# Kernel tuning notes

Hardware: AMD Instinct MI355X
Metric: run time of the kernel (lower is better)

The kernel has to match this reference:

```python
import jax, jax.numpy as jnp
import numpy as np

N_NODES = 50000
N_EDGES = 800000
LN_EPS = 1e-5


def _segment_softmax_aggr(msg, t, dst, n):
    # SoftmaxAggregation(learn=True): alpha = softmax(msg * t) per dest segment, out = sum(alpha * msg)
    logits = msg * t  # [E, C]
    m = jax.ops.segment_max(logits, dst, num_segments=n)
    m = jnp.where(jnp.isfinite(m), m, 0.0)  # empty segments -> 0 to keep exp finite
    e = jnp.exp(logits - m[dst])
    denom = jax.ops.segment_sum(e, dst, num_segments=n)
    alpha = e / jnp.maximum(denom[dst], 1e-16)
    return jax.ops.segment_sum(alpha * msg, dst, num_segments=n)


def _sage_conv(x, src, dst, wp, bp, t, wl, bl, wr):
    # project=True: messages come from relu(lin(x)); root term uses ORIGINAL x
    xp = jax.nn.relu(x @ wp + bp)
    msg = xp[src]                                   # [E, C] gather
    aggr = _segment_softmax_aggr(msg, t, dst, x.shape[0])
    out = aggr @ wl + bl + x @ wr
    # normalize=True: L2 normalize rows (eps as in F.normalize)
    nrm = jnp.maximum(jnp.linalg.norm(out, axis=-1, keepdims=True), 1e-12)
    return out / nrm


def _mem_pool(x, k, w_conv, wl, bl):
    # PyG MemPooling, tau=1: Student-t kernel 1/(1+d^2)
    H, K, F = k.shape
    kk = k.reshape(H * K, F)
    d2 = (jnp.sum(kk * kk, -1)[:, None] + jnp.sum(x * x, -1)[None, :]
          - 2.0 * kk @ x.T)                          # [H*K, N]
    d2 = jnp.maximum(d2, 0.0)
    dist = 1.0 / (1.0 + d2)
    dist = dist.reshape(H, K, -1).transpose(0, 2, 1)  # [H, N, K]
    S = dist / jnp.sum(dist, -1, keepdims=True)       # per-head normalize over clusters
    S = jnp.einsum('h,hnk->nk', w_conv, S)            # 1x1 conv mixing heads (no bias)
    S = jax.nn.softmax(S, axis=-1)                    # [N, K]
    xp = S.T @ x                                      # [K, F]
    return xp @ wl + bl                               # [K, out]


def setup_inputs() -> dict:
    key = jax.random.key(0)
    ks = jax.random.split(key, 20)
    rn = lambda i, shp, s: jax.random.normal(ks[i], shp, dtype=jnp.float32) * s
    inp = {
        'x': rn(0, (N_NODES, 64), 1.0),
        'edge_index': jax.random.randint(ks[1], (2, N_EDGES), 0, N_NODES, dtype=jnp.int32),
        'w_proj1': rn(2, (64, 64), 0.1), 'b_proj1': rn(3, (64,), 0.05),
        't1': jnp.ones((64,), jnp.float32),
        'w_l1': rn(4, (64, 256), 0.1), 'b_l1': rn(5, (256,), 0.05),
        'w_r1': rn(6, (64, 256), 0.1),
        'w_proj2': rn(7, (256, 256), 0.05), 'b_proj2': rn(8, (256,), 0.05),
        't2': jnp.ones((256,), jnp.float32),
        'w_l2': rn(9, (256, 128), 0.05), 'b_l2': rn(10, (128,), 0.05),
        'w_r2': rn(11, (256, 128), 0.05),
        'k_mem': rn(12, (4, 4, 128), 1.0),
        'w_conv': rn(13, (4,), 0.5),
        'w_memlin': rn(14, (128, 128), 0.08), 'b_memlin': rn(15, (128,), 0.05),
        'w_fx': rn(16, (128, 64), 0.08), 'b_fx': rn(17, (64,), 0.05),
        'gamma': jnp.ones((64,), jnp.float32),
        'beta': jnp.zeros((64,), jnp.float32),
    }
    return inp


def reference(x, edge_index, w_proj1, b_proj1, t1, w_l1, b_l1, w_r1,
              w_proj2, b_proj2, t2, w_l2, b_l2, w_r2,
              k_mem, w_conv, w_memlin, b_memlin, w_fx, b_fx, gamma, beta):
    src, dst = edge_index[0], edge_index[1]
    h = _sage_conv(x, src, dst, w_proj1, b_proj1, t1, w_l1, b_l1, w_r1)
    h = jax.nn.relu(h)                              # dropout = identity (eval)
    h = _sage_conv(h, src, dst, w_proj2, b_proj2, t2, w_l2, b_l2, w_r2)
    h = jax.nn.relu(h)
    pooled = _mem_pool(h, k_mem, w_conv, w_memlin, b_memlin)  # [4, 128]
    g = jnp.mean(pooled, axis=0, keepdims=True)     # global_mean_pool -> [1, 128]
    y = g @ w_fx + b_fx                             # [1, 64]
    mu = jnp.mean(y, -1, keepdims=True)
    var = jnp.var(y, -1, keepdims=True)
    y = (y - mu) / jnp.sqrt(var + LN_EPS) * gamma + beta
    return jax.nn.relu(y)
```

## Files before the change

### kernel.cpp

```cpp
#include <hip/hip_runtime.h>
#include <hip/hip_bf16.h>

#define N_NODES 50000
#define N_EDGES 800000
#define NB 196
#define PC_SLICES 2048

typedef __attribute__((ext_vector_type(8))) short short8;
typedef __attribute__((ext_vector_type(4))) float f32x4;
typedef __attribute__((ext_vector_type(2))) float f32x2;

#define QSCALE (2.f / 255.f)
#define QINV   127.5f

__device__ __forceinline__ float us2f(unsigned short u) {
    return __uint_as_float(((unsigned int)u) << 16);
}
__device__ __forceinline__ unsigned short f2bu(float f) {
    unsigned int u = __float_as_uint(f);
    unsigned int r = (u + 0x7fffu + ((u >> 16) & 1u)) >> 16;
    return (unsigned short)r;
}
__device__ __forceinline__ float exp2_hw(float x) {
    float r;
    __asm__("v_exp_f32 %0, %1" : "=v"(r) : "v"(x));
    return r;
}
#define LOG2E 1.44269504088896f

__global__ void k_hist(const int* __restrict__ dst, int* __restrict__ counts) {
    int e = blockIdx.x * 256 + threadIdx.x;
    if (e < N_EDGES) atomicAdd(&counts[dst[e]], 1);
}

__global__ __launch_bounds__(256) void k_scan1(const int* __restrict__ counts,
                                               int* __restrict__ row_ptr,
                                               int* __restrict__ partial) {
    __shared__ int sd[256];
    int t = threadIdx.x, i = blockIdx.x * 256 + t;
    int v = (i < N_NODES) ? counts[i] : 0;
    sd[t] = v;
    __syncthreads();
    for (int off = 1; off < 256; off <<= 1) {
        int o = (t >= off) ? sd[t - off] : 0;
        __syncthreads();
        sd[t] += o;
        __syncthreads();
    }
    if (i < N_NODES) row_ptr[i] = sd[t] - v;
    if (t == 255) partial[blockIdx.x] = sd[255];
}

__global__ __launch_bounds__(256) void k_scan2(int* __restrict__ partial,
                                               int* __restrict__ row_ptr) {
    __shared__ int sd[256];
    int t = threadIdx.x;
    int v = (t < NB) ? partial[t] : 0;
    sd[t] = v;
    __syncthreads();
    for (int off = 1; off < 256; off <<= 1) {
        int o = (t >= off) ? sd[t - off] : 0;
        __syncthreads();
        sd[t] += o;
        __syncthreads();
    }
    if (t < NB) partial[t] = sd[t] - v;
    if (t == NB - 1) row_ptr[N_NODES] = sd[t];
}

__global__ __launch_bounds__(256) void k_scan3(int* __restrict__ row_ptr,
                                               const int* __restrict__ partial,
                                               int* __restrict__ cursor) {
    int i = blockIdx.x * 256 + threadIdx.x;
    if (i < N_NODES) {
        int v = row_ptr[i] + partial[blockIdx.x];
        row_ptr[i] = v;
        cursor[i] = v;
    }
}

__global__ void k_scatter(const int* __restrict__ src, const int* __restrict__ dst,
                          int* __restrict__ cursor, int* __restrict__ src_sorted) {
    int e = blockIdx.x * 256 + threadIdx.x;
    if (e < N_EDGES) {
        int d = dst[e];
        int pos = atomicAdd(&cursor[d], 1);
        src_sorted[pos] = src[e];
    }
}

#define XCAST_N (N_NODES * 64)
__global__ __launch_bounds__(256) void k_prep(const float* __restrict__ x,
                                              const float* __restrict__ wp1,
                                              const float* __restrict__ wl1,
                                              const float* __restrict__ wr1,
                                              const float* __restrict__ wp2,
                                              const float* __restrict__ wl2,
                                              const float* __restrict__ wr2,
                                              unsigned short* __restrict__ cat1,
                                              unsigned short* __restrict__ B0T,
                                              unsigned short* __restrict__ B1T,
                                              unsigned short* __restrict__ BP2T,
                                              unsigned short* __restrict__ B2T) {
    int idx = blockIdx.x * 256 + threadIdx.x;
    if (idx < XCAST_N) {
        int i = idx >> 6, j = idx & 63;
        cat1[i * 128 + 64 + j] = f2bu(x[idx]);
        return;
    }
    int w = idx - XCAST_N;
    if (w < 4096)  { int k = w >> 6, n = w & 63;  B0T[n * 64 + k] = f2bu(wp1[w]); return; }
    w -= 4096;
    if (w < 16384) { int k = w >> 8, n = w & 255; B1T[n * 128 + k] = f2bu(wl1[w]); return; }
    w -= 16384;
    if (w < 16384) { int k = w >> 8, n = w & 255; B1T[n * 128 + 64 + k] = f2bu(wr1[w]); return; }
    w -= 16384;
    if (w < 65536) { int k = w >> 8, n = w & 255; BP2T[n * 256 + k] = f2bu(wp2[w]); return; }
    w -= 65536;
    if (w < 32768) { int k = w >> 7, n = w & 127; B2T[n * 512 + k] = f2bu(wl2[w]); return; }
    w -= 32768;
    if (w < 32768) { int k = w >> 7, n = w & 127; B2T[n * 512 + 256 + k] = f2bu(wr2[w]); return; }
}

template<int K, int C, int LDA, int LDOUT, int OUT_OFF, int EP, int WPB>
__global__ __launch_bounds__(256, WPB) void k_gemm(const unsigned short* __restrict__ A,
                                                   const unsigned short* __restrict__ BT,
                                                   const float* __restrict__ bias,
                                                   void* __restrict__ outv) {
    constexpr int NT = C / 16;
    constexpr int SAE = 128 * 72;
    constexpr int SBE = C * 72;
    constexpr int STAGE_B = (SAE + SBE) * 2;
    constexpr int RP_B = 64 * C * (EP == 2 ? 4 : (EP == 3 ? 1 : 2));
    constexpr int SMEM_B = STAGE_B > RP_B ? STAGE_B : RP_B;
    __shared__ __align__(16) char smem[SMEM_B];
    unsigned short* sA = (unsigned short*)smem;
    unsigned short* sB = sA + SAE;

    int t = threadIdx.x;
    int wid = t >> 6, lane = t & 63;
    int lrow = lane & 15, quad = lane >> 4;
    int m0 = blockIdx.x * 128;

    f32x4 acc[2][NT];
#pragma unroll
    for (int h = 0; h < 2; ++h)
#pragma unroll
        for (int nt = 0; nt < NT; ++nt)
#pragma unroll
            for (int r = 0; r < 4; ++r) acc[h][nt][r] = 0.f;

    for (int k0 = 0; k0 < K; k0 += 64) {
        __syncthreads();
        for (int i = t; i < 1024; i += 256) {
            int r = i >> 3, seg = i & 7;
            int m = m0 + r;
            uint4 v = make_uint4(0u, 0u, 0u, 0u);
            if (m < N_NODES) v = *(const uint4*)&A[(size_t)m * LDA + k0 + seg * 8];
            *(uint4*)&sA[r * 72 + seg * 8] = v;
        }
        for (int i = t; i < C * 8; i += 256) {
            int n = i >> 3, seg = i & 7;
            uint4 v = *(const uint4*)&BT[(size_t)n * K + k0 + seg * 8];
            *(uint4*)&sB[n * 72 + seg * 8] = v;
        }
        __syncthreads();
#pragma unroll
        for (int kk = 0; kk < 2; ++kk) {
            short8 a0 = *(const short8*)&sA[(wid * 16 + lrow) * 72 + kk * 32 + quad * 8];
            short8 a1 = *(const short8*)&sA[(64 + wid * 16 + lrow) * 72 + kk * 32 + quad * 8];
#pragma unroll
            for (int nt = 0; nt < NT; ++nt) {
                short8 bfg = *(const short8*)&sB[(nt * 16 + lrow) * 72 + kk * 32 + quad * 8];
                acc[0][nt] = __builtin_amdgcn_mfma_f32_16x16x32_bf16(a0, bfg, acc[0][nt], 0, 0, 0);
                acc[1][nt] = __builtin_amdgcn_mfma_f32_16x16x32_bf16(a1, bfg, acc[1][nt], 0, 0, 0);
            }
        }
    }

#pragma unroll
    for (int h = 0; h < 2; ++h) {
#pragma unroll
        for (int nt = 0; nt < NT; ++nt) {
            float bv = bias[nt * 16 + lrow];
#pragma unroll
            for (int r = 0; r < 4; ++r) acc[h][nt][r] += bv;
        }
        if (EP == 1 || EP == 2) {
#pragma unroll
            for (int r = 0; r < 4; ++r) {
                float ss = 0.f;
#pragma unroll
                for (int nt = 0; nt < NT; ++nt) ss += acc[h][nt][r] * acc[h][nt][r];
                ss += __shfl_xor(ss, 1);
                ss += __shfl_xor(ss, 2);
                ss += __shfl_xor(ss, 4);
                ss += __shfl_xor(ss, 8);
                float rinv = 1.f / fmaxf(sqrtf(ss), 1e-12f);
#pragma unroll
                for (int nt = 0; nt < NT; ++nt)
                    acc[h][nt][r] = fmaxf(acc[h][nt][r] * rinv, 0.f);
            }
        } else {
#pragma unroll
            for (int nt = 0; nt < NT; ++nt)
#pragma unroll
                for (int r = 0; r < 4; ++r) acc[h][nt][r] = fmaxf(acc[h][nt][r], 0.f);
        }
    }

    __syncthreads();
#pragma unroll
    for (int h = 0; h < 2; ++h) {
        if (EP == 2) {
            float* rp = (float*)smem;
#pragma unroll
            for (int nt = 0; nt < NT; ++nt)
#pragma unroll
                for (int r = 0; r < 4; ++r)
                    rp[(wid * 16 + quad * 4 + r) * C + nt * 16 + lrow] = acc[h][nt][r];
            __syncthreads();
            float* outp = (float*)outv;
            for (int i = t; i < 64 * C / 4; i += 256) {
                int f = i * 4, r = f / C, c = f % C;
                int m = m0 + h * 64 + r;
                if (m < N_NODES)
                    *(float4*)&outp[(size_t)m * LDOUT + OUT_OFF + c] = *(const float4*)&rp[f];
            }
            __syncthreads();
        } else if (EP == 3) {
            unsigned char* rp = (unsigned char*)smem;
#pragma unroll
            for (int nt = 0; nt < NT; ++nt)
#pragma unroll
                for (int r = 0; r < 4; ++r) {
                    float q = fminf(__builtin_rintf(acc[h][nt][r] * QINV), 255.f);
                    rp[(wid * 16 + quad * 4 + r) * C + nt * 16 + lrow] = (unsigned char)(int)q;
                }
            __syncthreads();
            unsigned char* outp = (unsigned char*)outv;
            for (int i = t; i < 64 * C / 16; i += 256) {
                int f = i * 16, r = f / C, c = f % C;
                int m = m0 + h * 64 + r;
                if (m < N_NODES)
                    *(uint4*)&outp[(size_t)m * LDOUT + OUT_OFF + c] = *(const uint4*)&rp[f];
            }
            __syncthreads();
        } else {
            unsigned short* rp = (unsigned short*)smem;
#pragma unroll
            for (int nt = 0; nt < NT; ++nt)
#pragma unroll
                for (int r = 0; r < 4; ++r)
                    rp[(wid * 16 + quad * 4 + r) * C + nt * 16 + lrow] = f2bu(acc[h][nt][r]);
            __syncthreads();
            unsigned short* outp = (unsigned short*)outv;
            for (int i = t; i < 64 * C / 8; i += 256) {
                int f = i * 8, r = f / C, c = f % C;
                int m = m0 + h * 64 + r;
                if (m < N_NODES)
                    *(uint4*)&outp[(size_t)m * LDOUT + OUT_OFF + c] = *(const uint4*)&rp[f];
            }
            __syncthreads();
        }
    }
}

__global__ __launch_bounds__(64) void k_aggr256(const unsigned char* __restrict__ xp,
                                                const float* __restrict__ tvec,
                                                const int* __restrict__ row_ptr,
                                                const int* __restrict__ srcs,
                                                unsigned short* __restrict__ outp) {
    int t = threadIdx.x;
    float4 tv4 = *(const float4*)&tvec[t * 4];
    f32x2 tv01 = {tv4.x * (LOG2E * QSCALE), tv4.y * (LOG2E * QSCALE)};
    f32x2 tv23 = {tv4.z * (LOG2E * QSCALE), tv4.w * (LOG2E * QSCALE)};
    int n = blockIdx.x;
    int beg = row_ptr[n], end = row_ptr[n + 1];
    f32x2 se01 = {0.f, 0.f}, se23 = {0.f, 0.f};
    f32x2 sem01 = {0.f, 0.f}, sem23 = {0.f, 0.f};
    int e = beg;
#define EDGE_BODY(VV, MSK)                                                     \
    {                                                                          \
        f32x2 m01 = {(float)((VV) & 0xFFu), (float)(((VV) >> 8) & 0xFFu)};     \
        f32x2 m23 = {(float)(((VV) >> 16) & 0xFFu), (float)((VV) >> 24)};      \
        f32x2 l01 = m01 * tv01, l23 = m23 * tv23;                              \
        f32x2 w01, w23;                                                        \
        w01.x = exp2_hw(l01.x) * (MSK); w01.y = exp2_hw(l01.y) * (MSK);        \
        w23.x = exp2_hw(l23.x) * (MSK); w23.y = exp2_hw(l23.y) * (MSK);        \
        se01 += w01; se23 += w23;                                              \
        sem01 = __builtin_elementwise_fma(w01, m01, sem01);                    \
        sem23 = __builtin_elementwise_fma(w23, m23, sem23);                    \
    }
    for (; e + 16 <= end; e += 16) {
        unsigned int v[16];
#pragma unroll
        for (int j = 0; j < 16; ++j) {
            const unsigned char* p = xp + (size_t)srcs[e + j] * 256;
            v[j] = *(const unsigned int*)&p[t * 4];
        }
#pragma unroll
        for (int j = 0; j < 16; ++j) EDGE_BODY(v[j], 1.f)
    }
    for (; e + 8 <= end; e += 8) {
        unsigned int v[8];
#pragma unroll
        for (int j = 0; j < 8; ++j) {
            const unsigned char* p = xp + (size_t)srcs[e + j] * 256;
            v[j] = *(const unsigned int*)&p[t * 4];
        }
#pragma unroll
        for (int j = 0; j < 8; ++j) EDGE_BODY(v[j], 1.f)
    }
    if (e < end) {
        int last = end - 1;
        unsigned int v[8];
#pragma unroll
        for (int j = 0; j < 8; ++j) {
            int ee = e + j;
            ee = ee < end ? ee : last;
            const unsigned char* p = xp + (size_t)srcs[ee] * 256;
            v[j] = *(const unsigned int*)&p[t * 4];
        }
#pragma unroll
        for (int j = 0; j < 8; ++j) {
            float msk = (e + j < end) ? 1.f : 0.f;
            EDGE_BODY(v[j], msk)
        }
    }
#undef EDGE_BODY
    ushort4 o;
    o.x = f2bu(QSCALE * sem01.x / fmaxf(se01.x, 1e-16f));
    o.y = f2bu(QSCALE * sem01.y / fmaxf(se01.y, 1e-16f));
    o.z = f2bu(QSCALE * sem23.x / fmaxf(se23.x, 1e-16f));
    o.w = f2bu(QSCALE * sem23.y / fmaxf(se23.y, 1e-16f));
    *(ushort4*)&outp[(size_t)n * 512 + t * 4] = o;
}

__global__ __launch_bounds__(64) void k_aggr64(const unsigned short* __restrict__ xp,
                                               const float* __restrict__ tvec,
                                               const int* __restrict__ row_ptr,
                                               const int* __restrict__ srcs,
                                               unsigned short* __restrict__ outp) {
    int c = threadIdx.x;
    float tv = tvec[c] * LOG2E;
    int n = blockIdx.x;
    int beg = row_ptr[n], end = row_ptr[n + 1];
    float se = 0.f, sem = 0.f;
    int e = beg;
    for (; e + 16 <= end; e += 16) {
        unsigned short v[16];
#pragma unroll
        for (int j = 0; j < 16; ++j)
            v[j] = xp[(size_t)srcs[e + j] * 64 + c];
#pragma unroll
        for (int j = 0; j < 16; ++j) {
            float msg = us2f(v[j]);
            float w = exp2_hw(msg * tv);
            se += w;
            sem = fmaf(w, msg, sem);
        }
    }
    for (; e + 8 <= end; e += 8) {
        unsigned short v[8];
#pragma unroll
        for (int j = 0; j < 8; ++j)
            v[j] = xp[(size_t)srcs[e + j] * 64 + c];
#pragma unroll
        for (int j = 0; j < 8; ++j) {
            float msg = us2f(v[j]);
            float w = exp2_hw(msg * tv);
            se += w;
            sem = fmaf(w, msg, sem);
        }
    }
    if (e < end) {
        int last = end - 1;
        unsigned short v[8];
#pragma unroll
        for (int j = 0; j < 8; ++j) {
            int ee = e + j;
            ee = ee < end ? ee : last;
            v[j] = xp[(size_t)srcs[ee] * 64 + c];
        }
#pragma unroll
        for (int j = 0; j < 8; ++j) {
            float msk = (e + j < end) ? 1.f : 0.f;
            float msg = us2f(v[j]);
            float w = exp2_hw(msg * tv) * msk;
            se += w;
            sem = fmaf(w, msg, sem);
        }
    }
    outp[(size_t)n * 128 + c] = f2bu(sem / fmaxf(se, 1e-16f));
}

__global__ __launch_bounds__(64) void k_pool_s(const float* __restrict__ h2,
                                               const float* __restrict__ kmem,
                                               const float* __restrict__ wconv,
                                               float* __restrict__ S) {
    __shared__ float kls[2048];
    __shared__ float kk2s[16];
    int t = threadIdx.x;
    for (int i = t; i < 2048; i += 64) kls[i] = kmem[i];
    __syncthreads();
    if (t < 16) {
        float s = 0.f;
        for (int f = 0; f < 128; ++f) { float v = kls[t * 128 + f]; s += v * v; }
        kk2s[t] = s;
    }
    __syncthreads();
    int n = blockIdx.x * 64 + t;
    if (n >= N_NODES) return;
    float dots[16];
#pragma unroll
    for (int k = 0; k < 16; ++k) dots[k] = 0.f;
    float x2 = 0.f;
    for (int c = 0; c < 32; ++c) {
        float4 xv = *(const float4*)&h2[(size_t)n * 128 + c * 4];
        x2 += xv.x * xv.x + xv.y * xv.y + xv.z * xv.z + xv.w * xv.w;
#pragma unroll
        for (int k = 0; k < 16; ++k) {
            float4 kv = *(const float4*)&kls[k * 128 + c * 4];
            dots[k] += xv.x * kv.x + xv.y * kv.y + xv.z * kv.z + xv.w * kv.w;
        }
    }
    float dist[16];
#pragma unroll
    for (int k = 0; k < 16; ++k) {
        float d2 = fmaxf(kk2s[k] + x2 - 2.f * dots[k], 0.f);
        dist[k] = 1.f / (1.f + d2);
    }
    float s0 = 0.f, s1 = 0.f, s2 = 0.f, s3 = 0.f;
#pragma unroll
    for (int h = 0; h < 4; ++h) {
        float den = dist[h * 4] + dist[h * 4 + 1] + dist[h * 4 + 2] + dist[h * 4 + 3];
        float inv = wconv[h] / den;
        s0 += dist[h * 4 + 0] * inv;
        s1 += dist[h * 4 + 1] * inv;
        s2 += dist[h * 4 + 2] * inv;
        s3 += dist[h * 4 + 3] * inv;
    }
    float mx = fmaxf(fmaxf(s0, s1), fmaxf(s2, s3));
    float e0 = __expf(s0 - mx), e1 = __expf(s1 - mx), e2 = __expf(s2 - mx), e3 = __expf(s3 - mx);
    float inv = 1.f / (e0 + e1 + e2 + e3);
    float4 o = make_float4(e0 * inv, e1 * inv, e2 * inv, e3 * inv);
    *(float4*)&S[(size_t)n * 4] = o;
}

__global__ __launch_bounds__(256) void k_pool_c(const float* __restrict__ h2,
                                                const float* __restrict__ Sm,
                                                float* __restrict__ part) {
    int t = threadIdx.x;
    int c = t & 127, sub = t >> 7;
    int slice = blockIdx.x * 2 + sub;
    float a0 = 0.f, a1 = 0.f, a2 = 0.f, a3 = 0.f;
    for (int n = slice; n < N_NODES; n += PC_SLICES) {
        float xv = h2[(size_t)n * 128 + c];
        float4 sv = *(const float4*)&Sm[(size_t)n * 4];
        a0 = fmaf(sv.x, xv, a0);
        a1 = fmaf(sv.y, xv, a1);
        a2 = fmaf(sv.z, xv, a2);
        a3 = fmaf(sv.w, xv, a3);
    }
    float* p = &part[(size_t)slice * 512];
    p[0 * 128 + c] = a0;
    p[1 * 128 + c] = a1;
    p[2 * 128 + c] = a2;
    p[3 * 128 + c] = a3;
}

__global__ __launch_bounds__(256) void k_pool_b(const float* __restrict__ part,
                                                float* __restrict__ pooled) {
    int j = blockIdx.x;
    float s = 0.f;
    for (int b = threadIdx.x; b < PC_SLICES; b += 256) s += part[(size_t)b * 512 + j];
#pragma unroll
    for (int off = 32; off > 0; off >>= 1) s += __shfl_xor(s, off);
    __shared__ float red[4];
    int lane = threadIdx.x & 63, wid = threadIdx.x >> 6;
    if (lane == 0) red[wid] = s;
    __syncthreads();
    if (threadIdx.x == 0) pooled[j] = red[0] + red[1] + red[2] + red[3];
}

__global__ __launch_bounds__(128) void k_final(const float* __restrict__ pooled,
                                               const float* __restrict__ wmem,
                                               const float* __restrict__ bmem,
                                               const float* __restrict__ wfx,
                                               const float* __restrict__ bfx,
                                               const float* __restrict__ gamma,
                                               const float* __restrict__ beta,
                                               float* __restrict__ out) {
    __shared__ float gx[128], g[128];
    int t = threadIdx.x;
    gx[t] = 0.25f * (pooled[t] + pooled[128 + t] + pooled[256 + t] + pooled[384 + t]);
    __syncthreads();
    float acc = bmem[t];
    for (int f = 0; f < 128; ++f) acc = fmaf(gx[f], wmem[f * 128 + t], acc);
    g[t] = acc;
    __syncthreads();
    if (t < 64) {
        float y = bfx[t];
        for (int f = 0; f < 128; ++f) y = fmaf(g[f], wfx[f * 64 + t], y);
        float s = y, s2 = y * y;
#pragma unroll
        for (int off = 32; off > 0; off >>= 1) {
            s += __shfl_xor(s, off);
            s2 += __shfl_xor(s2, off);
        }
        float mu = s * (1.f / 64.f);
        float var = s2 * (1.f / 64.f) - mu * mu;
        float v = (y - mu) / sqrtf(var + 1e-5f) * gamma[t] + beta[t];
        out[t] = fmaxf(v, 0.f);
    }
}

extern "C" void kernel_launch(void* const* d_in, const int* in_sizes, int n_in,
                              void* d_out, int out_size, void* d_ws, size_t ws_size,
                              hipStream_t stream) {
    const float* x        = (const float*)d_in[0];
    const int*   ei       = (const int*)  d_in[1];
    const float* w_proj1  = (const float*)d_in[2];
    const float* b_proj1  = (const float*)d_in[3];
    const float* t1       = (const float*)d_in[4];
    const float* w_l1     = (const float*)d_in[5];
    const float* b_l1     = (const float*)d_in[6];
    const float* w_r1     = (const float*)d_in[7];
    const float* w_proj2  = (const float*)d_in[8];
    const float* b_proj2  = (const float*)d_in[9];
    const float* t2       = (const float*)d_in[10];
    const float* w_l2     = (const float*)d_in[11];
    const float* b_l2     = (const float*)d_in[12];
    const float* w_r2     = (const float*)d_in[13];
    const float* k_mem    = (const float*)d_in[14];
    const float* w_conv   = (const float*)d_in[15];
    const float* w_memlin = (const float*)d_in[16];
    const float* b_memlin = (const float*)d_in[17];
    const float* w_fx     = (const float*)d_in[18];
    const float* b_fx     = (const float*)d_in[19];
    const float* gamma    = (const float*)d_in[20];
    const float* beta     = (const float*)d_in[21];
    const int* src = ei;
    const int* dst = ei + N_EDGES;
    (void)in_sizes; (void)n_in; (void)out_size; (void)ws_size;

    char* W = (char*)d_ws;
    const size_t MB = 1024 * 1024;
    int*   row_ptr    = (int*)(W + 0);
    int*   cursor     = (int*)(W + 256 * 1024);
    int*   partial    = (int*)(W + 512 * 1024);
    int*   src_sorted = (int*)(W + 768 * 1024);
    unsigned short* cat1 = (unsigned short*)(W + 4 * MB);
    unsigned short* xp1  = (unsigned short*)(W + 17 * MB);
    unsigned short* cat2 = (unsigned short*)(W + 24 * MB);
    unsigned char*  xp2  = (unsigned char*)(W + 76 * MB);
    float* h2     = (float*)(W + 102 * MB);
    float* Sm     = (float*)(W + 128 * MB);
    float* pooled = (float*)(W + 131 * MB);
    unsigned short* B0T  = (unsigned short*)(W + 133 * MB);
    unsigned short* B1T  = (unsigned short*)(W + 134 * MB);
    unsigned short* BP2T = (unsigned short*)(W + 135 * MB);
    unsigned short* B2T  = (unsigned short*)(W + 136 * MB);
    float* part   = (float*)(W + 140 * MB);

    hipMemsetAsync(cursor, 0, N_NODES * sizeof(int), stream);
    k_hist<<<(N_EDGES + 255) / 256, 256, 0, stream>>>(dst, cursor);
    k_scan1<<<NB, 256, 0, stream>>>(cursor, row_ptr, partial);
    k_scan2<<<1, 256, 0, stream>>>(partial, row_ptr);
    k_scan3<<<NB, 256, 0, stream>>>(row_ptr, partial, cursor);
    k_scatter<<<(N_EDGES + 255) / 256, 256, 0, stream>>>(src, dst, cursor, src_sorted);

    k_prep<<<(XCAST_N + 167936 + 255) / 256, 256, 0, stream>>>(
        x, w_proj1, w_l1, w_r1, w_proj2, w_l2, w_r2, cat1, B0T, B1T, BP2T, B2T);

    const int GB = (N_NODES + 127) / 128;

    k_gemm<64, 64, 128, 64, 0, 0, 4><<<GB, 256, 0, stream>>>(cat1 + 64, B0T, b_proj1, xp1);
    k_aggr64<<<N_NODES, 64, 0, stream>>>(xp1, t1, row_ptr, src_sorted, cat1);
    k_gemm<128, 256, 128, 512, 256, 1, 2><<<GB, 256, 0, stream>>>(cat1, B1T, b_l1, cat2);

    k_gemm<256, 256, 512, 256, 0, 3, 2><<<GB, 256, 0, stream>>>(cat2 + 256, BP2T, b_proj2, xp2);
    k_aggr256<<<N_NODES, 64, 0, stream>>>(xp2, t2, row_ptr, src_sorted, cat2);
    k_gemm<512, 128, 512, 128, 0, 2, 4><<<GB, 256, 0, stream>>>(cat2, B2T, b_l2, h2);

    k_pool_s<<<(N_NODES + 63) / 64, 64, 0, stream>>>(h2, k_mem, w_conv, Sm);
    k_pool_c<<<PC_SLICES / 2, 256, 0, stream>>>(h2, Sm, part);
    k_pool_b<<<512, 256, 0, stream>>>(part, pooled);
    k_final<<<1, 128, 0, stream>>>(pooled, w_memlin, b_memlin, w_fx, b_fx, gamma, beta,
                                   (float*)d_out);
}
```

Measured before the change: 388.8 us.

## Fuse pooling assignment into final GEMM epilogue and merge scan kernels

Computes the MemPooling soft assignment S directly from the fp32 result tile held in shared memory inside the last GEMM's epilogue. This removes the separate k_pool_s kernel and its full re-read of h2. It also folds the single-block partial scan into the per-block offset kernel, where each block reduces the preceding partial sums itself, and hardcodes the row_ptr tail as N_EDGES. The cost is extra shared memory and a lower occupancy hint (WPB 4 to 3) for that GEMM, plus redundant per-block reductions in the scan.

Result: no change. 385.7 us (-0.8%).

```diff
diff --git a/kernel.cpp b/kernel.cpp
--- a/kernel.cpp
+++ b/kernel.cpp
@@ -51,32 +51,25 @@
     if (t == 255) partial[blockIdx.x] = sd[255];
 }
 
-__global__ __launch_bounds__(256) void k_scan2(int* __restrict__ partial,
-                                               int* __restrict__ row_ptr) {
+__global__ __launch_bounds__(256) void k_scan3b(int* __restrict__ row_ptr,
+                                                const int* __restrict__ partial,
+                                                int* __restrict__ cursor) {
     __shared__ int sd[256];
     int t = threadIdx.x;
-    int v = (t < NB) ? partial[t] : 0;
-    sd[t] = v;
+    sd[t] = (t < blockIdx.x) ? partial[t] : 0;
     __syncthreads();
-    for (int off = 1; off < 256; off <<= 1) {
-        int o = (t >= off) ? sd[t - off] : 0;
+    for (int off = 128; off > 0; off >>= 1) {
+        if (t < off) sd[t] += sd[t + off];
         __syncthreads();
-        sd[t] += o;
-        __syncthreads();
-    }
-    if (t < NB) partial[t] = sd[t] - v;
-    if (t == NB - 1) row_ptr[N_NODES] = sd[t];
-}
-
-__global__ __launch_bounds__(256) void k_scan3(int* __restrict__ row_ptr,
-                                               const int* __restrict__ partial,
-                                               int* __restrict__ cursor) {
-    int i = blockIdx.x * 256 + threadIdx.x;
+    }
+    int base = sd[0];
+    int i = blockIdx.x * 256 + t;
     if (i < N_NODES) {
-        int v = row_ptr[i] + partial[blockIdx.x];
+        int v = row_ptr[i] + base;
         row_ptr[i] = v;
         cursor[i] = v;
     }
+    if (blockIdx.x == 0 && t == 0) row_ptr[N_NODES] = N_EDGES;
 }
 
 __global__ void k_scatter(const int* __restrict__ src, const int* __restrict__ dst,
@@ -126,21 +119,39 @@
 __global__ __launch_bounds__(256, WPB) void k_gemm(const unsigned short* __restrict__ A,
                                                    const unsigned short* __restrict__ BT,
                                                    const float* __restrict__ bias,
-                                                   void* __restrict__ outv) {
+                                                   void* __restrict__ outv,
+                                                   const float* __restrict__ kmem,
+                                                   const float* __restrict__ wconv,
+                                                   float* __restrict__ Sm) {
     constexpr int NT = C / 16;
     constexpr int SAE = 128 * 72;
     constexpr int SBE = C * 72;
     constexpr int STAGE_B = (SAE + SBE) * 2;
     constexpr int RP_B = 64 * C * (EP == 2 ? 4 : (EP == 3 ? 1 : 2));
     constexpr int SMEM_B = STAGE_B > RP_B ? STAGE_B : RP_B;
-    __shared__ __align__(16) char smem[SMEM_B];
+    constexpr int POOL_B = (EP == 2) ? (2048 * 4 + 64 + 16) : 16;
+    __shared__ __align__(16) char smem[SMEM_B + POOL_B];
     unsigned short* sA = (unsigned short*)smem;
     unsigned short* sB = sA + SAE;
+    float* kls  = (float*)(smem + SMEM_B);
+    float* kk2s = kls + 2048;
+    float* wcs  = kk2s + 16;
 
     int t = threadIdx.x;
     int wid = t >> 6, lane = t & 63;
     int lrow = lane & 15, quad = lane >> 4;
     int m0 = blockIdx.x * 128;
+
+    if (EP == 2) {
+        for (int i = t; i < 2048; i += 256) kls[i] = kmem[i];
+        if (t < 4) wcs[t] = wconv[t];
+        __syncthreads();
+        if (t < 16) {
+            float s = 0.f;
+            for (int f = 0; f < 128; ++f) { float v = kls[t * 128 + f]; s += v * v; }
+            kk2s[t] = s;
+        }
+    }
 
     f32x4 acc[2][NT];
 #pragma unroll
@@ -226,6 +237,59 @@
                 int m = m0 + h * 64 + r;
                 if (m < N_NODES)
                     *(float4*)&outp[(size_t)m * LDOUT + OUT_OFF + c] = *(const float4*)&rp[f];
+            }
+            {
+                int row = t >> 2, p = t & 3;
+                int cbase = p * 32;
+                float dots[16];
+#pragma unroll
+                for (int k = 0; k < 16; ++k) dots[k] = 0.f;
+                float x2 = 0.f;
+#pragma unroll
+                for (int c4 = 0; c4 < 8; ++c4) {
+                    float4 xv = *(const float4*)&rp[row * C + cbase + c4 * 4];
+                    x2 += xv.x * xv.x + xv.y * xv.y + xv.z * xv.z + xv.w * xv.w;
+#pragma unroll
+                    for (int k = 0; k < 16; ++k) {
+                        float4 kv = *(const float4*)&kls[k * 128 + cbase + c4 * 4];
+                        dots[k] += xv.x * kv.x + xv.y * kv.y + xv.z * kv.z + xv.w * kv.w;
+                    }
+                }
+#pragma unroll
+                for (int k = 0; k < 16; ++k) {
+                    dots[k] += __shfl_xor(dots[k], 1);
+                    dots[k] += __shfl_xor(dots[k], 2);
+                }
+                x2 += __shfl_xor(x2, 1);
+                x2 += __shfl_xor(x2, 2);
+                if (p == 0) {
+                    int m = m0 + h * 64 + row;
+                    if (m < N_NODES) {
+                        float dist[16];
+#pragma unroll
+                        for (int k = 0; k < 16; ++k) {
+                            float d2 = fmaxf(kk2s[k] + x2 - 2.f * dots[k], 0.f);
+                            dist[k] = 1.f / (1.f + d2);
+                        }
+                        float s0 = 0.f, s1 = 0.f, s2 = 0.f, s3 = 0.f;
+#pragma unroll
+                        for (int hh = 0; hh < 4; ++hh) {
+                            float den = dist[hh * 4] + dist[hh * 4 + 1] +
+                                        dist[hh * 4 + 2] + dist[hh * 4 + 3];
+                            float inv = wcs[hh] / den;
+                            s0 += dist[hh * 4 + 0] * inv;
+                            s1 += dist[hh * 4 + 1] * inv;
+                            s2 += dist[hh * 4 + 2] * inv;
+                            s3 += dist[hh * 4 + 3] * inv;
+                        }
+                        float mx = fmaxf(fmaxf(s0, s1), fmaxf(s2, s3));
+                        float e0 = __expf(s0 - mx), e1 = __expf(s1 - mx);
+                        float e2 = __expf(s2 - mx), e3 = __expf(s3 - mx);
+                        float inv = 1.f / (e0 + e1 + e2 + e3);
+                        *(float4*)&Sm[(size_t)m * 4] =
+                            make_float4(e0 * inv, e1 * inv, e2 * inv, e3 * inv);
+                    }
+                }
             }
             __syncthreads();
         } else if (EP == 3) {
@@ -393,59 +457,6 @@
         }
     }
     outp[(size_t)n * 128 + c] = f2bu(sem / fmaxf(se, 1e-16f));
-}
-
-__global__ __launch_bounds__(64) void k_pool_s(const float* __restrict__ h2,
-                                               const float* __restrict__ kmem,
-                                               const float* __restrict__ wconv,
-                                               float* __restrict__ S) {
-    __shared__ float kls[2048];
-    __shared__ float kk2s[16];
-    int t = threadIdx.x;
-    for (int i = t; i < 2048; i += 64) kls[i] = kmem[i];
-    __syncthreads();
-    if (t < 16) {
-        float s = 0.f;
-        for (int f = 0; f < 128; ++f) { float v = kls[t * 128 + f]; s += v * v; }
-        kk2s[t] = s;
-    }
-    __syncthreads();
-    int n = blockIdx.x * 64 + t;
-    if (n >= N_NODES) return;
-    float dots[16];
-#pragma unroll
-    for (int k = 0; k < 16; ++k) dots[k] = 0.f;
-    float x2 = 0.f;
-    for (int c = 0; c < 32; ++c) {
-        float4 xv = *(const float4*)&h2[(size_t)n * 128 + c * 4];
-        x2 += xv.x * xv.x + xv.y * xv.y + xv.z * xv.z + xv.w * xv.w;
-#pragma unroll
-        for (int k = 0; k < 16; ++k) {
-            float4 kv = *(const float4*)&kls[k * 128 + c * 4];
-            dots[k] += xv.x * kv.x + xv.y * kv.y + xv.z * kv.z + xv.w * kv.w;
-        }
-    }
-    float dist[16];
-#pragma unroll
-    for (int k = 0; k < 16; ++k) {
-        float d2 = fmaxf(kk2s[k] + x2 - 2.f * dots[k], 0.f);
-        dist[k] = 1.f / (1.f + d2);
-    }
-    float s0 = 0.f, s1 = 0.f, s2 = 0.f, s3 = 0.f;
-#pragma unroll
-    for (int h = 0; h < 4; ++h) {
-        float den = dist[h * 4] + dist[h * 4 + 1] + dist[h * 4 + 2] + dist[h * 4 + 3];
-        float inv = wconv[h] / den;
-        s0 += dist[h * 4 + 0] * inv;
-        s1 += dist[h * 4 + 1] * inv;
-        s2 += dist[h * 4 + 2] * inv;
-        s3 += dist[h * 4 + 3] * inv;
-    }
-    float mx = fmaxf(fmaxf(s0, s1), fmaxf(s2, s3));
-    float e0 = __expf(s0 - mx), e1 = __expf(s1 - mx), e2 = __expf(s2 - mx), e3 = __expf(s3 - mx);
-    float inv = 1.f / (e0 + e1 + e2 + e3);
-    float4 o = make_float4(e0 * inv, e1 * inv, e2 * inv, e3 * inv);
-    *(float4*)&S[(size_t)n * 4] = o;
 }
 
 __global__ __launch_bounds__(256) void k_pool_c(const float* __restrict__ h2,
@@ -567,8 +578,7 @@
     hipMemsetAsync(cursor, 0, N_NODES * sizeof(int), stream);
     k_hist<<<(N_EDGES + 255) / 256, 256, 0, stream>>>(dst, cursor);
     k_scan1<<<NB, 256, 0, stream>>>(cursor, row_ptr, partial);
-    k_scan2<<<1, 256, 0, stream>>>(partial, row_ptr);
-    k_scan3<<<NB, 256, 0, stream>>>(row_ptr, partial, cursor);
+    k_scan3b<<<NB, 256, 0, stream>>>(row_ptr, partial, cursor);
     k_scatter<<<(N_EDGES + 255) / 256, 256, 0, stream>>>(src, dst, cursor, src_sorted);
 
     k_prep<<<(XCAST_N + 167936 + 255) / 256, 256, 0, stream>>>(
@@ -576,15 +586,18 @@
 
     const int GB = (N_NODES + 127) / 128;
 
-    k_gemm<64, 64, 128, 64, 0, 0, 4><<<GB, 256, 0, stream>>>(cat1 + 64, B0T, b_proj1, xp1);
+    k_gemm<64, 64, 128, 64, 0, 0, 4><<<GB, 256, 0, stream>>>(
+        cat1 + 64, B0T, b_proj1, xp1, nullptr, nullptr, nullptr);
     k_aggr64<<<N_NODES, 64, 0, stream>>>(xp1, t1, row_ptr, src_sorted, cat1);
-    k_gemm<128, 256, 128, 512, 256, 1, 2><<<GB, 256, 0, stream>>>(cat1, B1T, b_l1, cat2);
-
-    k_gemm<256, 256, 512, 256, 0, 3, 2><<<GB, 256, 0, stream>>>(cat2 + 256, BP2T, b_proj2, xp2);
+    k_gemm<128, 256, 128, 512, 256, 1, 2><<<GB, 256, 0, stream>>>(
+        cat1, B1T, b_l1, cat2, nullptr, nullptr, nullptr);
+
+    k_gemm<256, 256, 512, 256, 0, 3, 2><<<GB, 256, 0, stream>>>(
+        cat2 + 256, BP2T, b_proj2, xp2, nullptr, nullptr, nullptr);
     k_aggr256<<<N_NODES, 64, 0, stream>>>(xp2, t2, row_ptr, src_sorted, cat2);
-    k_gemm<512, 128, 512, 128, 0, 2, 4><<<GB, 256, 0, stream>>>(cat2, B2T, b_l2, h2);
-
-    k_pool_s<<<(N_NODES + 63) / 64, 64, 0, stream>>>(h2, k_mem, w_conv, Sm);
+    k_gemm<512, 128, 512, 128, 0, 2, 3><<<GB, 256, 0, stream>>>(
+        cat2, B2T, b_l2, h2, k_mem, w_conv, Sm);
+
     k_pool_c<<<PC_SLICES / 2, 256, 0, stream>>>(h2, Sm, part);
     k_pool_b<<<512, 256, 0, stream>>>(part, pooled);
     k_final<<<1, 128, 0, stream>>>(pooled, w_memlin, b_memlin, w_fx, b_fx, gamma, beta,
```
